# Kernel optimization log

Hardware: AMD Instinct MI355X
Metric: run time of the kernel (lower is better)

The kernel has to match this reference:

```python
import jax, jax.numpy as jnp
import numpy as np

N = 100000
E = 1600000
HEADS = 4
C = 32  # per-head channels; HEADS*C = 128
NEG_SLOPE = 0.2
EPS = 1e-16


def gat_conv(x, src, dst, W, a_src, a_dst, b):
    """One PyG-style GATConv layer (concat=True, self loops already in src/dst).
    x: [N, F_in], W: [F_in, HEADS*C], a_src/a_dst: [HEADS, C], b: [HEADS*C].
    """
    h = (x @ W).reshape(N, HEADS, C)                 # [N, H, C]
    alpha_s = jnp.einsum('nhc,hc->nh', h, a_src)     # [N, H]
    alpha_d = jnp.einsum('nhc,hc->nh', h, a_dst)     # [N, H]
    e = alpha_s[src] + alpha_d[dst]                  # [E, H]
    e = jnp.where(e > 0, e, NEG_SLOPE * e)           # leaky_relu(0.2)
    # segment softmax over incoming edges of each dst node
    m = jax.ops.segment_max(e, dst, num_segments=N)  # [N, H]
    m = jnp.where(jnp.isfinite(m), m, 0.0)
    ex = jnp.exp(e - m[dst])                         # [E, H]
    denom = jax.ops.segment_sum(ex, dst, num_segments=N)
    alpha = ex / (denom[dst] + EPS)                  # [E, H]
    out = jax.ops.segment_sum(alpha[:, :, None] * h[src], dst, num_segments=N)
    return out.reshape(N, HEADS * C) + b


def setup_inputs() -> dict:
    key = jax.random.key(0)
    ks = jax.random.split(key, 6)
    x = jax.random.normal(ks[0], (N, 128), dtype=jnp.float32)
    edge_index = jax.random.randint(ks[1], (2, E), 0, N, dtype=jnp.int64)
    Ws = jax.random.normal(ks[2], (3, 128, 128), dtype=jnp.float32) * 0.1
    att_src = jax.random.normal(ks[3], (3, HEADS, C), dtype=jnp.float32) * 0.1
    att_dst = jax.random.normal(ks[4], (3, HEADS, C), dtype=jnp.float32) * 0.1
    bias = jnp.zeros((3, 128), dtype=jnp.float32)
    return {"x": x, "edge_index": edge_index, "Ws": Ws,
            "att_src": att_src, "att_dst": att_dst, "bias": bias}


def reference(x, edge_index, Ws, att_src, att_dst, bias):
    # PyG GATConv default add_self_loops=True: append i->i edges once.
    loops = jnp.arange(N, dtype=edge_index.dtype)
    src = jnp.concatenate([edge_index[0], loops])
    dst = jnp.concatenate([edge_index[1], loops])
    h = x
    n_layers = Ws.shape[0]
    for l in range(n_layers):
        h = gat_conv(h, src, dst, Ws[l], att_src[l], att_dst[l], bias[l])
        if l < n_layers - 1:
            h = jax.nn.relu(h)  # dropout p given but module run in eval -> identity
    return h
```

## Files before the change

### kernel.cpp

```cpp
#include <hip/hip_runtime.h>

#define HEADS 4
#define CPH 32
#define FDIM 128
#define NEG_SLOPE 0.2f
#define EPS_DEN 1e-16f

#define BSH 9
#define BKT (1 << BSH)
#define SCHUNK 4096


__global__ __launch_bounds__(256) void bucket_count_kernel(
        const int* __restrict__ ei, int* __restrict__ bcnt, int E, int N, int NB) {
    __shared__ int hist[512];
    int tid = threadIdx.x;
    int ET = E + N;
    for (int b = tid; b < 512; b += 256) hist[b] = 0;
    __syncthreads();
    int i = blockIdx.x * blockDim.x + tid;
    int stride = gridDim.x * blockDim.x;
    for (; i < ET; i += stride) {
        int d = (i < E) ? ei[E + i] : (i - E);
        atomicAdd(&hist[d >> BSH], 1);
    }
    __syncthreads();
    for (int b = tid; b < NB; b += 256) {
        int c = hist[b];
        if (c) atomicAdd(&bcnt[b], c);
    }
}

__global__ void bucket_scan_kernel(const int* __restrict__ bcnt, int* __restrict__ bbase,
                                   int* __restrict__ bcur, int NB,
                                   int* __restrict__ row_ptr, int N) {
    if (blockIdx.x == 0 && threadIdx.x == 0) {
        int run = 0;
        for (int b = 0; b < NB; ++b) { bbase[b] = run; bcur[b] = run; run += bcnt[b]; }
        bbase[NB] = run;
        row_ptr[N] = run;
    }
}

__global__ __launch_bounds__(256) void bucket_scatter_kernel(
        const int* __restrict__ ei, int* __restrict__ bcur, int2* __restrict__ pairs,
        int E, int N, int NB) {
    __shared__ int hist[512];
    __shared__ int lcur[512];
    int ET = E + N;
    int tid = threadIdx.x;
    for (int cbase = blockIdx.x * SCHUNK; cbase < ET; cbase += gridDim.x * SCHUNK) {
        int cend = min(cbase + SCHUNK, ET);
        for (int b = tid; b < NB; b += 256) hist[b] = 0;
        __syncthreads();
        for (int i = cbase + tid; i < cend; i += 256) {
            int d = (i < E) ? ei[E + i] : (i - E);
            atomicAdd(&hist[d >> BSH], 1);
        }
        __syncthreads();
        for (int b = tid; b < NB; b += 256) {
            int c = hist[b];
            lcur[b] = c ? atomicAdd(&bcur[b], c) : 0;
        }
        __syncthreads();
        for (int i = cbase + tid; i < cend; i += 256) {
            int s, d;
            if (i < E) { s = ei[i]; d = ei[E + i]; }
            else       { s = i - E; d = s; }
            int p = atomicAdd(&lcur[d >> BSH], 1);
            pairs[p] = make_int2(s, d);
        }
        __syncthreads();
    }
}

__global__ __launch_bounds__(256) void csr_from_buckets_kernel(
        const int2* __restrict__ pairs, const int* __restrict__ bbase,
        int* __restrict__ row_ptr, int* __restrict__ csr_src, int N) {
    __shared__ int hist[BKT];
    __shared__ int ssum[256];
    int b  = blockIdx.x;
    int lo = b << BSH;
    int hi = min(lo + BKT, N);
    int nn = hi - lo;
    int tid = threadIdx.x;
    for (int i = tid; i < BKT; i += 256) hist[i] = 0;
    __syncthreads();
    int s0 = bbase[b];
    int s1 = bbase[b + 1];
    for (int j = s0 + tid; j < s1; j += 256)
        atomicAdd(&hist[pairs[j].y - lo], 1);
    __syncthreads();
    int e0 = hist[2 * tid];
    int e1 = hist[2 * tid + 1];
    int ps = e0 + e1;
    ssum[tid] = ps;
    __syncthreads();
    for (int d = 1; d < 256; d <<= 1) {
        int v = ssum[tid];
        int u = (tid >= d) ? ssum[tid - d] : 0;
        __syncthreads();
        ssum[tid] = v + u;
        __syncthreads();
    }
    int excl = ssum[tid] - ps;
    int p0 = s0 + excl;
    int p1 = p0 + e0;
    if (2 * tid < nn)     row_ptr[lo + 2 * tid]     = p0;
    if (2 * tid + 1 < nn) row_ptr[lo + 2 * tid + 1] = p1;
    hist[2 * tid]     = p0;
    hist[2 * tid + 1] = p1;
    __syncthreads();
    for (int j = s0 + tid; j < s1; j += 256) {
        int2 pr = pairs[j];
        int p = atomicAdd(&hist[pr.y - lo], 1);
        csr_src[p] = pr.x;
    }
}

#define AS_LD 68

__global__ __launch_bounds__(256) void gemm_alpha_kernel(
        const float* __restrict__ X, const float* __restrict__ W,
        const float* __restrict__ a_src, const float* __restrict__ a_dst,
        float* __restrict__ H, float* __restrict__ ASo, float* __restrict__ ADo, int n) {
    __shared__ float As[32][AS_LD];
    __shared__ float Bs[32][128];
    int tid = threadIdx.x;
    int block_row = blockIdx.x * 64;
    int cg = tid & 15;
    int rg = tid >> 4;
    int r0 = rg * 4;
    int ca = cg * 4;
    int cb = 64 + cg * 4;

    int arow = tid >> 3;
    int akk  = (tid & 7) << 2;
    int bkr  = tid >> 5;
    int bc4  = (tid & 31) << 2;
    int ga0 = block_row + arow;
    int ga1 = ga0 + 32;
    const float4 f4z = make_float4(0.f, 0.f, 0.f, 0.f);
    float4 ra0, ra1, rb0, rb1, rb2, rb3;

    auto LOAD = [&](int k0) {
        ra0 = (ga0 < n) ? *(const float4*)&X[(size_t)ga0 * FDIM + k0 + akk] : f4z;
        ra1 = (ga1 < n) ? *(const float4*)&X[(size_t)ga1 * FDIM + k0 + akk] : f4z;
        rb0 = *(const float4*)&W[(size_t)(k0 + bkr     ) * FDIM + bc4];
        rb1 = *(const float4*)&W[(size_t)(k0 + bkr +  8) * FDIM + bc4];
        rb2 = *(const float4*)&W[(size_t)(k0 + bkr + 16) * FDIM + bc4];
        rb3 = *(const float4*)&W[(size_t)(k0 + bkr + 24) * FDIM + bc4];
    };
    auto STORE = [&]() {
        As[akk + 0][arow] = ra0.x; As[akk + 1][arow] = ra0.y;
        As[akk + 2][arow] = ra0.z; As[akk + 3][arow] = ra0.w;
        As[akk + 0][arow + 32] = ra1.x; As[akk + 1][arow + 32] = ra1.y;
        As[akk + 2][arow + 32] = ra1.z; As[akk + 3][arow + 32] = ra1.w;
        *(float4*)&Bs[bkr     ][bc4] = rb0;
        *(float4*)&Bs[bkr +  8][bc4] = rb1;
        *(float4*)&Bs[bkr + 16][bc4] = rb2;
        *(float4*)&Bs[bkr + 24][bc4] = rb3;
    };

    float acc[4][8];
#pragma unroll
    for (int i = 0; i < 4; ++i)
#pragma unroll
        for (int j = 0; j < 8; ++j) acc[i][j] = 0.f;

    LOAD(0);
    for (int c = 0; c < 4; ++c) {
        STORE();
        __syncthreads();
        if (c < 3) LOAD((c + 1) * 32);
#pragma unroll
        for (int k = 0; k < 32; ++k) {
            float4 a  = *(const float4*)&As[k][r0];
            float4 b1 = *(const float4*)&Bs[k][ca];
            float4 b2 = *(const float4*)&Bs[k][cb];
            float av[4] = {a.x, a.y, a.z, a.w};
            float bv[8] = {b1.x, b1.y, b1.z, b1.w, b2.x, b2.y, b2.z, b2.w};
#pragma unroll
            for (int i = 0; i < 4; ++i)
#pragma unroll
                for (int j = 0; j < 8; ++j) acc[i][j] = fmaf(av[i], bv[j], acc[i][j]);
        }
        __syncthreads();
    }

    int hd_a = cg >> 3;
    int hd_b = 2 + hd_a;
    int co = (cg & 7) * 4;
    float4 wsa = *(const float4*)&a_src[hd_a * CPH + co];
    float4 wsb = *(const float4*)&a_src[hd_b * CPH + co];
    float4 wda = *(const float4*)&a_dst[hd_a * CPH + co];
    float4 wdb = *(const float4*)&a_dst[hd_b * CPH + co];
#pragma unroll
    for (int i = 0; i < 4; ++i) {
        int grow = block_row + r0 + i;
        bool ok = grow < n;
        if (ok) {
            *(float4*)&H[(size_t)grow * FDIM + ca] =
                make_float4(acc[i][0], acc[i][1], acc[i][2], acc[i][3]);
            *(float4*)&H[(size_t)grow * FDIM + cb] =
                make_float4(acc[i][4], acc[i][5], acc[i][6], acc[i][7]);
        }
        float psa = acc[i][0] * wsa.x + acc[i][1] * wsa.y + acc[i][2] * wsa.z + acc[i][3] * wsa.w;
        float psb = acc[i][4] * wsb.x + acc[i][5] * wsb.y + acc[i][6] * wsb.z + acc[i][7] * wsb.w;
        float pda = acc[i][0] * wda.x + acc[i][1] * wda.y + acc[i][2] * wda.z + acc[i][3] * wda.w;
        float pdb = acc[i][4] * wdb.x + acc[i][5] * wdb.y + acc[i][6] * wdb.z + acc[i][7] * wdb.w;
#pragma unroll
        for (int off = 1; off <= 4; off <<= 1) {
            psa += __shfl_xor(psa, off);
            psb += __shfl_xor(psb, off);
            pda += __shfl_xor(pda, off);
            pdb += __shfl_xor(pdb, off);
        }
        if (ok && (cg & 7) == 0) {
            ASo[(size_t)grow * HEADS + hd_a] = psa;
            ASo[(size_t)grow * HEADS + hd_b] = psb;
            ADo[(size_t)grow * HEADS + hd_a] = pda;
            ADo[(size_t)grow * HEADS + hd_b] = pdb;
        }
    }
}

__global__ __launch_bounds__(256) void aggregate_kernel(
        const float* __restrict__ H, const float* __restrict__ ASi, const float* __restrict__ ADi,
        const int* __restrict__ row_ptr, const int* __restrict__ csr_src,
        const float* __restrict__ bias, float* __restrict__ OUT, int n, int relu) {
    __shared__ float4 xs[4][64];
    __shared__ int    ss[4][64];
    int wid = (int)((blockIdx.x * (size_t)blockDim.x + threadIdx.x) >> 6);
    if (wid >= n) return;
    int lane = threadIdx.x & 63;
    int wv   = (threadIdx.x >> 6) & 3;
    int half = lane >> 5;
    int lq   = lane & 31;
    int head = lq >> 3;
    int c0   = lq << 2;
    const float* xsf = (const float*)&xs[wv][0];

    int start = row_ptr[wid];
    int end   = row_ptr[wid + 1];
    float4 adv = *(const float4*)&ADi[(size_t)wid * HEADS];

    float m = -INFINITY;
    float dn = 0.f;
    float a0 = 0.f, a1 = 0.f, a2 = 0.f, a3 = 0.f;

    for (int base = start; base < end; base += 64) {
        int cnt = min(64, end - base);
        int idx = base + lane;
        float e0 = -INFINITY, e1 = -INFINITY, e2 = -INFINITY, e3 = -INFINITY;
        int my_src = 0;
        if (idx < end) {
            my_src = csr_src[idx];
            float4 as = *(const float4*)&ASi[(size_t)my_src * HEADS];
            float t;
            t = as.x + adv.x; e0 = t > 0.f ? t : NEG_SLOPE * t;
            t = as.y + adv.y; e1 = t > 0.f ? t : NEG_SLOPE * t;
            t = as.z + adv.z; e2 = t > 0.f ? t : NEG_SLOPE * t;
            t = as.w + adv.w; e3 = t > 0.f ? t : NEG_SLOPE * t;
        }
        float q0 = e0, q1 = e1, q2 = e2, q3 = e3;
#pragma unroll
        for (int off = 32; off; off >>= 1) {
            q0 = fmaxf(q0, __shfl_xor(q0, off));
            q1 = fmaxf(q1, __shfl_xor(q1, off));
            q2 = fmaxf(q2, __shfl_xor(q2, off));
            q3 = fmaxf(q3, __shfl_xor(q3, off));
        }
        float cm = head == 0 ? q0 : head == 1 ? q1 : head == 2 ? q2 : q3;
        float nm = fmaxf(m, cm);
        float s = __expf(m - nm);
        a0 *= s; a1 *= s; a2 *= s; a3 *= s; dn *= s;
        m = nm;
        float m0 = __shfl(m, 0), m1 = __shfl(m, 8), m2 = __shfl(m, 16), m3 = __shfl(m, 24);
        float x0 = __expf(e0 - m0);
        float x1 = __expf(e1 - m1);
        float x2 = __expf(e2 - m2);
        float x3 = __expf(e3 - m3);

        xs[wv][lane] = make_float4(x0, x1, x2, x3);
        ss[wv][lane] = my_src;
        __builtin_amdgcn_wave_barrier();

        int hs = (cnt + 1) >> 1;
        float4 va = make_float4(0.f, 0.f, 0.f, 0.f);
        float4 vb = make_float4(0.f, 0.f, 0.f, 0.f);
        int sA = half;
        if (sA < cnt) {
            int sidx = ss[wv][sA];
            va = *(const float4*)&H[(size_t)sidx * FDIM + c0];
        }
        int sB = half + 2;
        if (sB < cnt) {
            int sidx = ss[wv][sB];
            vb = *(const float4*)&H[(size_t)sidx * FDIM + c0];
        }
        for (int j = 0; j < hs; ++j) {
            int sc = 2 * j + half;
            float xh = xsf[sc * 4 + head];
            float4 cv = va;
            va = vb;
            int sn = sc + 4;
            if (sn < cnt) {
                int sidx = ss[wv][sn];
                vb = *(const float4*)&H[(size_t)sidx * FDIM + c0];
            }
            a0 = fmaf(xh, cv.x, a0);
            a1 = fmaf(xh, cv.y, a1);
            a2 = fmaf(xh, cv.z, a2);
            a3 = fmaf(xh, cv.w, a3);
            dn += xh;
        }
    }

    a0 += __shfl_xor(a0, 32);
    a1 += __shfl_xor(a1, 32);
    a2 += __shfl_xor(a2, 32);
    a3 += __shfl_xor(a3, 32);
    dn += __shfl_xor(dn, 32);

    if (half == 0) {
        float inv = 1.f / (dn + EPS_DEN);
        float4 bv = *(const float4*)&bias[c0];
        float o0 = fmaf(a0, inv, bv.x);
        float o1 = fmaf(a1, inv, bv.y);
        float o2 = fmaf(a2, inv, bv.z);
        float o3 = fmaf(a3, inv, bv.w);
        if (relu) {
            o0 = fmaxf(o0, 0.f); o1 = fmaxf(o1, 0.f);
            o2 = fmaxf(o2, 0.f); o3 = fmaxf(o3, 0.f);
        }
        *(float4*)&OUT[(size_t)wid * FDIM + c0] = make_float4(o0, o1, o2, o3);
    }
}


extern "C" void kernel_launch(void* const* d_in, const int* in_sizes, int n_in,
                              void* d_out, int out_size, void* d_ws, size_t ws_size,
                              hipStream_t stream) {
    const int N = in_sizes[0] / FDIM;
    const int E = in_sizes[1] / 2;
    const int NB = (N + BKT - 1) >> BSH;

    const float* x    = (const float*)d_in[0];
    const int*   ei   = (const int*)d_in[1];
    const float* Ws   = (const float*)d_in[2];
    const float* asrc = (const float*)d_in[3];
    const float* adst = (const float*)d_in[4];
    const float* bias = (const float*)d_in[5];
    float* out = (float*)d_out;

    char* w = (char*)d_ws;
    auto carve = [&](size_t bytes) -> void* {
        void* p = (void*)w;
        w += (bytes + 255) & ~(size_t)255;
        return p;
    };
    float* hA      = (float*)carve((size_t)N * FDIM * 4);
    float* hB      = (float*)carve((size_t)N * FDIM * 4);
    float* ASb     = (float*)carve((size_t)N * HEADS * 4);
    float* ADb     = (float*)carve((size_t)N * HEADS * 4);
    int*   row_ptr = (int*)carve((size_t)(N + 1) * 4);
    int*   csr_src = (int*)carve((size_t)(E + N) * 4);
    int*   bcnt    = (int*)carve(4096);
    int*   bbase   = (int*)carve(4096);
    int*   bcur    = (int*)carve(4096);
    int2*  pairs   = (int2*)hB;

    hipMemsetAsync(bcnt, 0, (size_t)NB * 4, stream);
    bucket_count_kernel<<<1024, 256, 0, stream>>>(ei, bcnt, E, N, NB);
    bucket_scan_kernel<<<1, 64, 0, stream>>>(bcnt, bbase, bcur, NB, row_ptr, N);
    int sblk = min(416, (E + N + SCHUNK - 1) / SCHUNK);
    bucket_scatter_kernel<<<sblk, 256, 0, stream>>>(ei, bcur, pairs, E, N, NB);
    csr_from_buckets_kernel<<<NB, 256, 0, stream>>>(pairs, bbase, row_ptr, csr_src, N);

    const float* X = x;
    for (int l = 0; l < 3; ++l) {
        gemm_alpha_kernel<<<(N + 63) / 64, 256, 0, stream>>>(
            X, Ws + (size_t)l * FDIM * FDIM, asrc + l * HEADS * CPH, adst + l * HEADS * CPH,
            hA, ASb, ADb, N);
        float* O = (l == 2) ? out : hB;
        aggregate_kernel<<<(N + 3) / 4, 256, 0, stream>>>(
            hA, ASb, ADb, row_ptr, csr_src, bias + (size_t)l * FDIM, O, N, (l < 2) ? 1 : 0);
        X = hB;
    }
}
```

Before: 749.8 us.

## Drop online-softmax max tracking and replace LDS staging with wave shuffles

```diff
diff --git a/kernel.cpp b/kernel.cpp
--- a/kernel.cpp
+++ b/kernel.cpp
@@ -229,23 +229,18 @@
         const float* __restrict__ H, const float* __restrict__ ASi, const float* __restrict__ ADi,
         const int* __restrict__ row_ptr, const int* __restrict__ csr_src,
         const float* __restrict__ bias, float* __restrict__ OUT, int n, int relu) {
-    __shared__ float4 xs[4][64];
-    __shared__ int    ss[4][64];
     int wid = (int)((blockIdx.x * (size_t)blockDim.x + threadIdx.x) >> 6);
     if (wid >= n) return;
     int lane = threadIdx.x & 63;
-    int wv   = (threadIdx.x >> 6) & 3;
     int half = lane >> 5;
     int lq   = lane & 31;
     int head = lq >> 3;
     int c0   = lq << 2;
-    const float* xsf = (const float*)&xs[wv][0];
 
     int start = row_ptr[wid];
     int end   = row_ptr[wid + 1];
     float4 adv = *(const float4*)&ADi[(size_t)wid * HEADS];
 
-    float m = -INFINITY;
     float dn = 0.f;
     float a0 = 0.f, a1 = 0.f, a2 = 0.f, a3 = 0.f;
 
@@ -263,50 +258,34 @@
             t = as.z + adv.z; e2 = t > 0.f ? t : NEG_SLOPE * t;
             t = as.w + adv.w; e3 = t > 0.f ? t : NEG_SLOPE * t;
         }
-        float q0 = e0, q1 = e1, q2 = e2, q3 = e3;
-#pragma unroll
-        for (int off = 32; off; off >>= 1) {
-            q0 = fmaxf(q0, __shfl_xor(q0, off));
-            q1 = fmaxf(q1, __shfl_xor(q1, off));
-            q2 = fmaxf(q2, __shfl_xor(q2, off));
-            q3 = fmaxf(q3, __shfl_xor(q3, off));
-        }
-        float cm = head == 0 ? q0 : head == 1 ? q1 : head == 2 ? q2 : q3;
-        float nm = fmaxf(m, cm);
-        float s = __expf(m - nm);
-        a0 *= s; a1 *= s; a2 *= s; a3 *= s; dn *= s;
-        m = nm;
-        float m0 = __shfl(m, 0), m1 = __shfl(m, 8), m2 = __shfl(m, 16), m3 = __shfl(m, 24);
-        float x0 = __expf(e0 - m0);
-        float x1 = __expf(e1 - m1);
-        float x2 = __expf(e2 - m2);
-        float x3 = __expf(e3 - m3);
-
-        xs[wv][lane] = make_float4(x0, x1, x2, x3);
-        ss[wv][lane] = my_src;
-        __builtin_amdgcn_wave_barrier();
+        float x0 = __expf(fminf(e0, 80.f));
+        float x1 = __expf(fminf(e1, 80.f));
+        float x2 = __expf(fminf(e2, 80.f));
+        float x3 = __expf(fminf(e3, 80.f));
 
         int hs = (cnt + 1) >> 1;
         float4 va = make_float4(0.f, 0.f, 0.f, 0.f);
         float4 vb = make_float4(0.f, 0.f, 0.f, 0.f);
         int sA = half;
         if (sA < cnt) {
-            int sidx = ss[wv][sA];
+            int sidx = __shfl(my_src, sA);
             va = *(const float4*)&H[(size_t)sidx * FDIM + c0];
         }
         int sB = half + 2;
         if (sB < cnt) {
-            int sidx = ss[wv][sB];
+            int sidx = __shfl(my_src, sB);
             vb = *(const float4*)&H[(size_t)sidx * FDIM + c0];
         }
         for (int j = 0; j < hs; ++j) {
             int sc = 2 * j + half;
-            float xh = xsf[sc * 4 + head];
+            float t0 = __shfl(x0, sc), t1 = __shfl(x1, sc);
+            float t2 = __shfl(x2, sc), t3 = __shfl(x3, sc);
+            float xh = head == 0 ? t0 : head == 1 ? t1 : head == 2 ? t2 : t3;
             float4 cv = va;
             va = vb;
             int sn = sc + 4;
             if (sn < cnt) {
-                int sidx = ss[wv][sn];
+                int sidx = __shfl(my_src, sn);
                 vb = *(const float4*)&H[(size_t)sidx * FDIM + c0];
             }
             a0 = fmaf(xh, cv.x, a0);
```

Result: no change. 754.7 us (+0.6%).
